# Optimization experiments

Hardware: AMD Instinct MI355X
Metric: run time of the kernel (lower is better)

The kernel has to match this reference:

```python
import jax, jax.numpy as jnp
import numpy as np

C = 64  # in_channels == out_channels (required by final view)

def setup_inputs() -> dict:
    key = jax.random.key(0)
    ks = jax.random.split(key, 7)
    x = jax.random.normal(ks[0], (2, C, 16, 16, 16), dtype=jnp.float32)
    s = 1.0 / np.sqrt(C)
    Wq = jax.random.uniform(ks[1], (C, C), jnp.float32, -s, s)
    bq = jax.random.uniform(ks[2], (C,), jnp.float32, -s, s)
    Wk = jax.random.uniform(ks[3], (C, C), jnp.float32, -s, s)
    bk = jax.random.uniform(ks[4], (C,), jnp.float32, -s, s)
    Wv = jax.random.uniform(ks[5], (C, C), jnp.float32, -s, s)
    bv = jax.random.uniform(ks[6], (C,), jnp.float32, -s, s)
    return {"x": x, "Wq": Wq, "bq": bq, "Wk": Wk, "bk": bk, "Wv": Wv, "bv": bv}

def _proj(x, W, b):
    # 1x1x1 Conv3d == per-voxel channel GEMM; x: [B,C,D,H,W]
    return jnp.einsum('oc,bcdhw->bodhw', W, x) + b[None, :, None, None, None]

def reference(x, Wq, bq, Wk, bk, Wv, bv):
    B, Cin, D, H, W = x.shape
    q = _proj(x, Wq, bq).reshape(B, C, -1)  # [B,C,N]
    k = _proj(x, Wk, bk).reshape(B, C, -1)
    v = _proj(x, Wv, bv).reshape(B, C, -1)
    # attention[b,i,j] = softmax_j(q_i . k_j); NOTE: unscaled, as in the source
    attn = jax.nn.softmax(jnp.einsum('bci,bcj->bij', q, k), axis=-1)
    out = jnp.einsum('bcj,bij->bci', v, attn)  # out_i = sum_j a_ij v_j
    return out.reshape(x.shape)
```

## Files before the change

### kernel.cpp

```cpp
#include <hip/hip_runtime.h>
#include <math.h>

#define CCH 64
#define NVOX 4096
#define NB 2
#define TS 136
#define SMAX 16.0f

typedef _Float16 f16x8 __attribute__((ext_vector_type(8)));
typedef _Float16 f16x4 __attribute__((ext_vector_type(4)));
typedef __fp16   g16x2 __attribute__((ext_vector_type(2)));
typedef float f32x4 __attribute__((ext_vector_type(4)));

__global__ __launch_bounds__(256) void qkv_proj(
    const float* __restrict__ x,
    const float* __restrict__ Wq, const float* __restrict__ bq,
    const float* __restrict__ Wk, const float* __restrict__ bk,
    const float* __restrict__ Wv, const float* __restrict__ bv,
    _Float16* __restrict__ qh, _Float16* __restrict__ khf, _Float16* __restrict__ vhf)
{
    __shared__ float Ws[3 * 64 * 64];
    __shared__ float xs[64 * 32];
    const int t  = threadIdx.x;
    const int b  = blockIdx.x >> 7;
    const int i0 = (blockIdx.x & 127) * 32;

    {
        const float4* Wq4 = (const float4*)Wq;
        const float4* Wk4 = (const float4*)Wk;
        const float4* Wv4 = (const float4*)Wv;
        float4* Ws4 = (float4*)Ws;
#pragma unroll
        for (int s = 0; s < 4; ++s) {
            int idx = t + 256 * s;
            Ws4[idx]        = Wq4[idx];
            Ws4[1024 + idx] = Wk4[idx];
            Ws4[2048 + idx] = Wv4[idx];
        }
    }
    {
        int cc = t >> 2;
        int m0 = (t & 3) * 8;
        const float* src = x + ((b * CCH + cc) * NVOX) + i0 + m0;
#pragma unroll
        for (int s = 0; s < 8; ++s) xs[cc * 32 + m0 + s] = src[s];
    }
    __syncthreads();

    const int vox = t & 31;
    const int c0  = (t >> 5) * 8;
    const int j   = i0 + vox;
    const int jb  = j >> 4;

#pragma unroll
    for (int m = 0; m < 3; ++m) {
        const float* Wm  = &Ws[m * 4096];
        const float* bia = (m == 0) ? bq : (m == 1) ? bk : bv;
        float acc[8];
#pragma unroll
        for (int jj = 0; jj < 8; ++jj) acc[jj] = bia[c0 + jj];
        for (int cc = 0; cc < 64; cc += 4) {
            float xv0 = xs[(cc + 0) * 32 + vox];
            float xv1 = xs[(cc + 1) * 32 + vox];
            float xv2 = xs[(cc + 2) * 32 + vox];
            float xv3 = xs[(cc + 3) * 32 + vox];
#pragma unroll
            for (int jj = 0; jj < 8; ++jj) {
                float4 w = *(const float4*)&Wm[(c0 + jj) * 64 + cc];
                acc[jj] = fmaf(w.x, xv0, acc[jj]);
                acc[jj] = fmaf(w.y, xv1, acc[jj]);
                acc[jj] = fmaf(w.z, xv2, acc[jj]);
                acc[jj] = fmaf(w.w, xv3, acc[jj]);
            }
        }
        if (m == 0) {
            f16x8 hv;
#pragma unroll
            for (int jj = 0; jj < 8; ++jj) hv[jj] = (_Float16)acc[jj];
            *(f16x8*)&qh[((size_t)(b * NVOX) + j) * CCH + c0] = hv;
        } else if (m == 1) {
            f16x8 hv;
#pragma unroll
            for (int jj = 0; jj < 8; ++jj) hv[jj] = (_Float16)acc[jj];
            const int ks = c0 >> 5, q4 = (c0 >> 3) & 3, n = j & 15;
            *(f16x8*)&khf[((((size_t)b * 256 + jb) * 2 + ks) * 64 + q4 * 16 + n) * 8] = hv;
        } else {
            const int q4v = (j >> 2) & 3, r = j & 3;
#pragma unroll
            for (int jj = 0; jj < 8; ++jj) {
                const int c = c0 + jj, mt = c >> 4, nch = c & 15;
                vhf[((((size_t)b * 256 + jb) * 4 + mt) * 64 + q4v * 16 + nch) * 4 + r] =
                    (_Float16)acc[jj];
            }
        }
    }
}

template <int SPLIT>
__global__ __launch_bounds__(256) void attn(
    const _Float16* __restrict__ qh, const _Float16* __restrict__ khf,
    const _Float16* __restrict__ vhf,
    _Float16* __restrict__ po,
    float* __restrict__ ml,
    float* __restrict__ out)
{
    __shared__ _Float16 tb[64 * TS];

    constexpr int LS = (SPLIT == 8) ? 3 : (SPLIT == 4) ? 2 : (SPLIT == 2) ? 1 : 0;
    const int t    = threadIdx.x;
    const int h    = blockIdx.x & (SPLIT - 1);
    const int tile = blockIdx.x >> LS;
    const int b    = tile >> 5;
    const int i0   = (tile & 31) * 128;

    const int lane = t & 63;
    const int w    = t >> 6;
    const int q4   = lane >> 4;
    const int n    = lane & 15;

    const int JT = 64 / SPLIT;
    const f16x8* k8 = (const f16x8*)khf;
    const f16x4* v4 = (const f16x4*)vhf;

    f16x8 aq[2][2];
#pragma unroll
    for (int g = 0; g < 2; ++g) {
        const _Float16* qrow =
            qh + ((size_t)(b * NVOX) + i0 + w * 32 + g * 16 + n) * CCH + q4 * 8;
        aq[g][0] = *(const f16x8*)(qrow);
        aq[g][1] = *(const f16x8*)(qrow + 32);
    }

    float l[2] = {0.f, 0.f};
    f32x4 o[2][4];
#pragma unroll
    for (int g = 0; g < 2; ++g)
#pragma unroll
        for (int mt = 0; mt < 4; ++mt) o[g][mt] = (f32x4){0.f, 0.f, 0.f, 0.f};

    f16x8 akA[2][4], akB[2][4];
    f16x4 av[4][4];

    auto loadK = [&](int jt, f16x8 (&ak)[2][4]) {
        const size_t jb0 = (size_t)b * 256 + (h * JT + jt) * 4;
#pragma unroll
        for (int nt = 0; nt < 4; ++nt)
#pragma unroll
            for (int ks = 0; ks < 2; ++ks)
                ak[ks][nt] = k8[((jb0 + nt) * 2 + ks) * 64 + lane];
    };
    auto loadV = [&](int jt) {
        const size_t jb0 = (size_t)b * 256 + (h * JT + jt) * 4;
#pragma unroll
        for (int nt = 0; nt < 4; ++nt)
#pragma unroll
            for (int mt = 0; mt < 4; ++mt)
                av[nt][mt] = v4[((jb0 + nt) * 4 + mt) * 64 + lane];
    };

    auto compute_tile = [&](const f16x8 (&ak)[2][4]) {
        f32x4 s[2][4];
#pragma unroll
        for (int g = 0; g < 2; ++g)
#pragma unroll
            for (int nt = 0; nt < 4; ++nt) s[g][nt] = (f32x4){0.f, 0.f, 0.f, 0.f};
#pragma unroll
        for (int ks = 0; ks < 2; ++ks)
#pragma unroll
            for (int nt = 0; nt < 4; ++nt) {
                s[0][nt] = __builtin_amdgcn_mfma_f32_16x16x32_f16(ak[ks][nt], aq[0][ks], s[0][nt], 0, 0, 0);
                s[1][nt] = __builtin_amdgcn_mfma_f32_16x16x32_f16(ak[ks][nt], aq[1][ks], s[1][nt], 0, 0, 0);
            }

        f16x4 bp[2][4];
#pragma unroll
        for (int g = 0; g < 2; ++g) {
#pragma unroll
            for (int nt = 0; nt < 4; ++nt) {
                float p0 = __expf(s[g][nt][0] - SMAX);
                float p1 = __expf(s[g][nt][1] - SMAX);
                float p2 = __expf(s[g][nt][2] - SMAX);
                float p3 = __expf(s[g][nt][3] - SMAX);
                l[g] += (p0 + p1) + (p2 + p3);
                union { g16x2 g2[2]; f16x4 h4; } u;
                u.g2[0] = __builtin_amdgcn_cvt_pkrtz(p0, p1);
                u.g2[1] = __builtin_amdgcn_cvt_pkrtz(p2, p3);
                bp[g][nt] = u.h4;
            }
        }

#pragma unroll
        for (int nt = 0; nt < 4; ++nt)
#pragma unroll
            for (int mt = 0; mt < 4; ++mt) {
                o[0][mt] = __builtin_amdgcn_mfma_f32_16x16x16f16(av[nt][mt], bp[0][nt], o[0][mt], 0, 0, 0);
                o[1][mt] = __builtin_amdgcn_mfma_f32_16x16x16f16(av[nt][mt], bp[1][nt], o[1][mt], 0, 0, 0);
            }
    };

    loadK(0, akA);
    for (int jt = 0; jt < JT; jt += 2) {
        loadV(jt);
        if (jt + 1 < JT) loadK(jt + 1, akB);
        compute_tile(akA);
        if (jt + 1 < JT) {
            loadV(jt + 1);
            if (jt + 2 < JT) loadK(jt + 2, akA);
            compute_tile(akB);
        }
    }

    float l_tot[2];
#pragma unroll
    for (int g = 0; g < 2; ++g) {
        float lv = l[g];
        lv += __shfl_xor(lv, 16, 64);
        lv += __shfl_xor(lv, 32, 64);
        l_tot[g] = lv;
    }

    if (SPLIT > 1) {
#pragma unroll
        for (int g = 0; g < 2; ++g)
#pragma unroll
            for (int mt = 0; mt < 4; ++mt)
#pragma unroll
                for (int r = 0; r < 4; ++r)
                    tb[(mt * 16 + q4 * 4 + r) * TS + w * 32 + g * 16 + n] =
                        (_Float16)o[g][mt][r];
#pragma unroll
        for (int g = 0; g < 2; ++g) {
            if (q4 == 0) {
                const int ig = i0 + w * 32 + g * 16 + n;
                float2* mlp = (float2*)&ml[((size_t)(b * SPLIT + h) * NVOX + ig) * 2];
                *mlp = make_float2(SMAX, l_tot[g]);
            }
        }
        __syncthreads();
        const int cr = t >> 2;
        const int ib = (t & 3) * 32;
        const size_t base = ((size_t)(b * SPLIT + h) * 64 + cr) * NVOX + i0 + ib;
#pragma unroll
        for (int u = 0; u < 4; ++u) {
            f16x8 vv = *(const f16x8*)&tb[cr * TS + ib + u * 8];
            *(f16x8*)&po[base + u * 8] = vv;
        }
    } else {
#pragma unroll
        for (int g = 0; g < 2; ++g) {
            const int ig = i0 + w * 32 + g * 16 + n;
            const float inv = 1.0f / l_tot[g];
#pragma unroll
            for (int mt = 0; mt < 4; ++mt)
#pragma unroll
                for (int r = 0; r < 4; ++r)
                    out[(size_t)(b * CCH + mt * 16 + q4 * 4 + r) * NVOX + ig] =
                        o[g][mt][r] * inv;
        }
    }
}

template <int SPLIT>
__global__ __launch_bounds__(256) void combine(
    const _Float16* __restrict__ po, const float* __restrict__ ml,
    float* __restrict__ out)
{
    __shared__ float wls[SPLIT * 32];
    const int t  = threadIdx.x;
    const int b  = blockIdx.x >> 7;
    const int i0 = (blockIdx.x & 127) * 32;

    if (t < 32) {
        const int i = i0 + t;
        float mv[SPLIT], lv[SPLIT], M = -1e30f;
#pragma unroll
        for (int h = 0; h < SPLIT; ++h) {
            mv[h] = ml[((size_t)(b * SPLIT + h) * NVOX + i) * 2 + 0];
            lv[h] = ml[((size_t)(b * SPLIT + h) * NVOX + i) * 2 + 1];
            M = fmaxf(M, mv[h]);
        }
        float den = 0.f;
#pragma unroll
        for (int h = 0; h < SPLIT; ++h) den += lv[h] * __expf(mv[h] - M);
        const float inv = 1.0f / den;
#pragma unroll
        for (int h = 0; h < SPLIT; ++h) wls[h * 32 + t] = __expf(mv[h] - M) * inv;
    }
    __syncthreads();

    const int c  = t >> 2;
    const int iq = t & 3;
    float acc[8];
#pragma unroll
    for (int e = 0; e < 8; ++e) acc[e] = 0.f;
#pragma unroll
    for (int h = 0; h < SPLIT; ++h) {
        f16x8 f = *(const f16x8*)&po[((size_t)(b * SPLIT + h) * 64 + c) * NVOX + i0 + iq * 8];
        const float* wp = &wls[h * 32 + iq * 8];
#pragma unroll
        for (int e = 0; e < 8; ++e)
            acc[e] = fmaf((float)f[e], wp[e], acc[e]);
    }
    float4* dst = (float4*)&out[(size_t)(b * CCH + c) * NVOX + i0 + iq * 8];
    dst[0] = make_float4(acc[0], acc[1], acc[2], acc[3]);
    dst[1] = make_float4(acc[4], acc[5], acc[6], acc[7]);
}

extern "C" void kernel_launch(void* const* d_in, const int* in_sizes, int n_in,
                              void* d_out, int out_size, void* d_ws, size_t ws_size,
                              hipStream_t stream)
{
    const float* x  = (const float*)d_in[0];
    const float* Wq = (const float*)d_in[1];
    const float* bq = (const float*)d_in[2];
    const float* Wk = (const float*)d_in[3];
    const float* bk = (const float*)d_in[4];
    const float* Wv = (const float*)d_in[5];
    const float* bv = (const float*)d_in[6];
    float* out = (float*)d_out;

    _Float16* qh  = (_Float16*)d_ws;
    _Float16* khf = qh + NB * NVOX * CCH;
    _Float16* vhf = khf + NB * NVOX * CCH;
    _Float16* po  = vhf + NB * NVOX * CCH;
    const size_t qkv_bytes = (size_t)3 * NB * NVOX * CCH * sizeof(_Float16);

    qkv_proj<<<NB * (NVOX / 32), 256, 0, stream>>>(x, Wq, bq, Wk, bk, Wv, bv, qh, khf, vhf);

    auto need = [&](int sp) {
        return qkv_bytes + (size_t)NB * sp * 64 * NVOX * sizeof(_Float16)
                         + (size_t)NB * sp * NVOX * 2 * sizeof(float);
    };

    if (ws_size >= need(8)) {
        float* ml = (float*)(po + (size_t)NB * 8 * 64 * NVOX);
        attn<8><<<NB * 32 * 8, 256, 0, stream>>>(qh, khf, vhf, po, ml, out);
        combine<8><<<NB * 128, 256, 0, stream>>>(po, ml, out);
    } else if (ws_size >= need(4)) {
        float* ml = (float*)(po + (size_t)NB * 4 * 64 * NVOX);
        attn<4><<<NB * 32 * 4, 256, 0, stream>>>(qh, khf, vhf, po, ml, out);
        combine<4><<<NB * 128, 256, 0, stream>>>(po, ml, out);
    } else if (ws_size >= need(2)) {
        float* ml = (float*)(po + (size_t)NB * 2 * 64 * NVOX);
        attn<2><<<NB * 32 * 2, 256, 0, stream>>>(qh, khf, vhf, po, ml, out);
        combine<2><<<NB * 128, 256, 0, stream>>>(po, ml, out);
    } else {
        attn<1><<<NB * 32, 256, 0, stream>>>(qh, khf, vhf, nullptr, nullptr, out);
    }
}
```

Baseline: 103.5 us.

## Halve attention query tile per block and drop K double-buffering

Each attention block now covers 64 query rows instead of 128 (one 16-row group per wave), which doubles the grid size. The explicit K register double-buffering is replaced by a simple loop that loads K and V together each tile. The aim is fewer registers per thread, giving higher occupancy and more blocks to spread across CUs. The cost is that every K/V tile is loaded twice as often in total, and there is less manual overlap of loads with MFMA work.

After: 110.1 us. 1.06x slower.

```diff
diff --git a/kernel.cpp b/kernel.cpp
--- a/kernel.cpp
+++ b/kernel.cpp
@@ -4,7 +4,7 @@
 #define CCH 64
 #define NVOX 4096
 #define NB 2
-#define TS 136
+#define TS 72
 #define SMAX 16.0f
 
 typedef _Float16 f16x8 __attribute__((ext_vector_type(8)));
@@ -110,8 +110,8 @@
     const int t    = threadIdx.x;
     const int h    = blockIdx.x & (SPLIT - 1);
     const int tile = blockIdx.x >> LS;
-    const int b    = tile >> 5;
-    const int i0   = (tile & 31) * 128;
+    const int b    = tile >> 6;
+    const int i0   = (tile & 63) * 64;
 
     const int lane = t & 63;
     const int w    = t >> 6;
@@ -122,141 +122,95 @@
     const f16x8* k8 = (const f16x8*)khf;
     const f16x4* v4 = (const f16x4*)vhf;
 
-    f16x8 aq[2][2];
-#pragma unroll
-    for (int g = 0; g < 2; ++g) {
+    f16x8 aq[2];
+    {
         const _Float16* qrow =
-            qh + ((size_t)(b * NVOX) + i0 + w * 32 + g * 16 + n) * CCH + q4 * 8;
-        aq[g][0] = *(const f16x8*)(qrow);
-        aq[g][1] = *(const f16x8*)(qrow + 32);
-    }
-
-    float l[2] = {0.f, 0.f};
-    f32x4 o[2][4];
-#pragma unroll
-    for (int g = 0; g < 2; ++g)
-#pragma unroll
-        for (int mt = 0; mt < 4; ++mt) o[g][mt] = (f32x4){0.f, 0.f, 0.f, 0.f};
-
-    f16x8 akA[2][4], akB[2][4];
-    f16x4 av[4][4];
-
-    auto loadK = [&](int jt, f16x8 (&ak)[2][4]) {
+            qh + ((size_t)(b * NVOX) + i0 + w * 16 + n) * CCH + q4 * 8;
+        aq[0] = *(const f16x8*)(qrow);
+        aq[1] = *(const f16x8*)(qrow + 32);
+    }
+
+    float l = 0.f;
+    f32x4 o[4];
+#pragma unroll
+    for (int mt = 0; mt < 4; ++mt) o[mt] = (f32x4){0.f, 0.f, 0.f, 0.f};
+
+    for (int jt = 0; jt < JT; ++jt) {
         const size_t jb0 = (size_t)b * 256 + (h * JT + jt) * 4;
+
+        f16x8 ak[2][4];
+        f16x4 av[4][4];
 #pragma unroll
         for (int nt = 0; nt < 4; ++nt)
 #pragma unroll
             for (int ks = 0; ks < 2; ++ks)
                 ak[ks][nt] = k8[((jb0 + nt) * 2 + ks) * 64 + lane];
-    };
-    auto loadV = [&](int jt) {
-        const size_t jb0 = (size_t)b * 256 + (h * JT + jt) * 4;
 #pragma unroll
         for (int nt = 0; nt < 4; ++nt)
 #pragma unroll
             for (int mt = 0; mt < 4; ++mt)
                 av[nt][mt] = v4[((jb0 + nt) * 4 + mt) * 64 + lane];
-    };
-
-    auto compute_tile = [&](const f16x8 (&ak)[2][4]) {
-        f32x4 s[2][4];
-#pragma unroll
-        for (int g = 0; g < 2; ++g)
-#pragma unroll
-            for (int nt = 0; nt < 4; ++nt) s[g][nt] = (f32x4){0.f, 0.f, 0.f, 0.f};
+
+        f32x4 s[4];
+#pragma unroll
+        for (int nt = 0; nt < 4; ++nt) s[nt] = (f32x4){0.f, 0.f, 0.f, 0.f};
 #pragma unroll
         for (int ks = 0; ks < 2; ++ks)
 #pragma unroll
-            for (int nt = 0; nt < 4; ++nt) {
-                s[0][nt] = __builtin_amdgcn_mfma_f32_16x16x32_f16(ak[ks][nt], aq[0][ks], s[0][nt], 0, 0, 0);
-                s[1][nt] = __builtin_amdgcn_mfma_f32_16x16x32_f16(ak[ks][nt], aq[1][ks], s[1][nt], 0, 0, 0);
-            }
-
-        f16x4 bp[2][4];
-#pragma unroll
-        for (int g = 0; g < 2; ++g) {
-#pragma unroll
-            for (int nt = 0; nt < 4; ++nt) {
-                float p0 = __expf(s[g][nt][0] - SMAX);
-                float p1 = __expf(s[g][nt][1] - SMAX);
-                float p2 = __expf(s[g][nt][2] - SMAX);
-                float p3 = __expf(s[g][nt][3] - SMAX);
-                l[g] += (p0 + p1) + (p2 + p3);
-                union { g16x2 g2[2]; f16x4 h4; } u;
-                u.g2[0] = __builtin_amdgcn_cvt_pkrtz(p0, p1);
-                u.g2[1] = __builtin_amdgcn_cvt_pkrtz(p2, p3);
-                bp[g][nt] = u.h4;
-            }
+            for (int nt = 0; nt < 4; ++nt)
+                s[nt] = __builtin_amdgcn_mfma_f32_16x16x32_f16(ak[ks][nt], aq[ks], s[nt], 0, 0, 0);
+
+        f16x4 bp[4];
+#pragma unroll
+        for (int nt = 0; nt < 4; ++nt) {
+            float p0 = __expf(s[nt][0] - SMAX);
+            float p1 = __expf(s[nt][1] - SMAX);
+            float p2 = __expf(s[nt][2] - SMAX);
+            float p3 = __expf(s[nt][3] - SMAX);
+            l += (p0 + p1) + (p2 + p3);
+            union { g16x2 g2[2]; f16x4 h4; } u;
+            u.g2[0] = __builtin_amdgcn_cvt_pkrtz(p0, p1);
+            u.g2[1] = __builtin_amdgcn_cvt_pkrtz(p2, p3);
+            bp[nt] = u.h4;
         }
 
 #pragma unroll
         for (int nt = 0; nt < 4; ++nt)
 #pragma unroll
-            for (int mt = 0; mt < 4; ++mt) {
-                o[0][mt] = __builtin_amdgcn_mfma_f32_16x16x16f16(av[nt][mt], bp[0][nt], o[0][mt], 0, 0, 0);
-                o[1][mt] = __builtin_amdgcn_mfma_f32_16x16x16f16(av[nt][mt], bp[1][nt], o[1][mt], 0, 0, 0);
-            }
-    };
-
-    loadK(0, akA);
-    for (int jt = 0; jt < JT; jt += 2) {
-        loadV(jt);
-        if (jt + 1 < JT) loadK(jt + 1, akB);
-        compute_tile(akA);
-        if (jt + 1 < JT) {
-            loadV(jt + 1);
-            if (jt + 2 < JT) loadK(jt + 2, akA);
-            compute_tile(akB);
-        }
-    }
-
-    float l_tot[2];
-#pragma unroll
-    for (int g = 0; g < 2; ++g) {
-        float lv = l[g];
-        lv += __shfl_xor(lv, 16, 64);
-        lv += __shfl_xor(lv, 32, 64);
-        l_tot[g] = lv;
-    }
+            for (int mt = 0; mt < 4; ++mt)
+                o[mt] = __builtin_amdgcn_mfma_f32_16x16x16f16(av[nt][mt], bp[nt], o[mt], 0, 0, 0);
+    }
+
+    float l_tot = l;
+    l_tot += __shfl_xor(l_tot, 16, 64);
+    l_tot += __shfl_xor(l_tot, 32, 64);
 
     if (SPLIT > 1) {
 #pragma unroll
-        for (int g = 0; g < 2; ++g)
-#pragma unroll
-            for (int mt = 0; mt < 4; ++mt)
-#pragma unroll
-                for (int r = 0; r < 4; ++r)
-                    tb[(mt * 16 + q4 * 4 + r) * TS + w * 32 + g * 16 + n] =
-                        (_Float16)o[g][mt][r];
-#pragma unroll
-        for (int g = 0; g < 2; ++g) {
-            if (q4 == 0) {
-                const int ig = i0 + w * 32 + g * 16 + n;
-                float2* mlp = (float2*)&ml[((size_t)(b * SPLIT + h) * NVOX + ig) * 2];
-                *mlp = make_float2(SMAX, l_tot[g]);
-            }
+        for (int mt = 0; mt < 4; ++mt)
+#pragma unroll
+            for (int r = 0; r < 4; ++r)
+                tb[(mt * 16 + q4 * 4 + r) * TS + w * 16 + n] = (_Float16)o[mt][r];
+        if (q4 == 0) {
+            const int ig = i0 + w * 16 + n;
+            float2* mlp = (float2*)&ml[((size_t)(b * SPLIT + h) * NVOX + ig) * 2];
+            *mlp = make_float2(SMAX, l_tot);
         }
         __syncthreads();
         const int cr = t >> 2;
-        const int ib = (t & 3) * 32;
+        const int ib = (t & 3) * 16;
         const size_t base = ((size_t)(b * SPLIT + h) * 64 + cr) * NVOX + i0 + ib;
-#pragma unroll
-        for (int u = 0; u < 4; ++u) {
-            f16x8 vv = *(const f16x8*)&tb[cr * TS + ib + u * 8];
-            *(f16x8*)&po[base + u * 8] = vv;
-        }
+        *(f16x8*)&po[base]     = *(const f16x8*)&tb[cr * TS + ib];
+        *(f16x8*)&po[base + 8] = *(const f16x8*)&tb[cr * TS + ib + 8];
     } else {
-#pragma unroll
-        for (int g = 0; g < 2; ++g) {
-            const int ig = i0 + w * 32 + g * 16 + n;
-            const float inv = 1.0f / l_tot[g];
-#pragma unroll
-            for (int mt = 0; mt < 4; ++mt)
-#pragma unroll
-                for (int r = 0; r < 4; ++r)
-                    out[(size_t)(b * CCH + mt * 16 + q4 * 4 + r) * NVOX + ig] =
-                        o[g][mt][r] * inv;
-        }
+        const int ig = i0 + w * 16 + n;
+        const float inv = 1.0f / l_tot;
+#pragma unroll
+        for (int mt = 0; mt < 4; ++mt)
+#pragma unroll
+            for (int r = 0; r < 4; ++r)
+                out[(size_t)(b * CCH + mt * 16 + q4 * 4 + r) * NVOX + ig] =
+                    o[mt][r] * inv;
     }
 }
 
@@ -334,17 +288,17 @@
 
     if (ws_size >= need(8)) {
         float* ml = (float*)(po + (size_t)NB * 8 * 64 * NVOX);
-        attn<8><<<NB * 32 * 8, 256, 0, stream>>>(qh, khf, vhf, po, ml, out);
+        attn<8><<<NB * 64 * 8, 256, 0, stream>>>(qh, khf, vhf, po, ml, out);
         combine<8><<<NB * 128, 256, 0, stream>>>(po, ml, out);
     } else if (ws_size >= need(4)) {
         float* ml = (float*)(po + (size_t)NB * 4 * 64 * NVOX);
-        attn<4><<<NB * 32 * 4, 256, 0, stream>>>(qh, khf, vhf, po, ml, out);
+        attn<4><<<NB * 64 * 4, 256, 0, stream>>>(qh, khf, vhf, po, ml, out);
         combine<4><<<NB * 128, 256, 0, stream>>>(po, ml, out);
     } else if (ws_size >= need(2)) {
         float* ml = (float*)(po + (size_t)NB * 2 * 64 * NVOX);
-        attn<2><<<NB * 32 * 2, 256, 0, stream>>>(qh, khf, vhf, po, ml, out);
+        attn<2><<<NB * 64 * 2, 256, 0, stream>>>(qh, khf, vhf, po, ml, out);
         combine<2><<<NB * 128, 256, 0, stream>>>(po, ml, out);
     } else {
-        attn<1><<<NB * 32, 256, 0, stream>>>(qh, khf, vhf, nullptr, nullptr, out);
+        attn<1><<<NB * 64, 256, 0, stream>>>(qh, khf, vhf, nullptr, nullptr, out);
     }
 }
```
